# Kernel optimization log

Measured on AMD Instinct MI355X. Metric: run time of the kernel, lower is better.

Reference implementation:

```python
import jax, jax.numpy as jnp
import numpy as np

NEG_SLOPE = 0.2  # PyG GATConv default negative_slope
LN_EPS = 1e-5


def gat_conv(x, edge, W, a_src, a_dst, bias, concat):
    """PyG-style GATConv. edge: [2, E] (src, dst), self-loops already included."""
    H, C = a_src.shape
    n = x.shape[0]
    xh = (x @ W).reshape(n, H, C)                      # [N, H, C]
    es = jnp.einsum('nhc,hc->nh', xh, a_src)           # [N, H]
    ed = jnp.einsum('nhc,hc->nh', xh, a_dst)           # [N, H]
    src, dst = edge[0], edge[1]
    e = jax.nn.leaky_relu(es[src] + ed[dst], NEG_SLOPE)  # [E, H]
    m = jax.ops.segment_max(e, dst, num_segments=n)      # [N, H]
    m = jnp.where(jnp.isfinite(m), m, 0.0)
    w = jnp.exp(e - m[dst])                              # [E, H]
    denom = jax.ops.segment_sum(w, dst, num_segments=n)  # [N, H] (>0: self-loops)
    alpha = w / denom[dst]                               # [E, H]
    out = jax.ops.segment_sum(alpha[:, :, None] * xh[src], dst, num_segments=n)  # [N,H,C]
    out = out.reshape(n, H * C) if concat else out.mean(axis=1)
    return out + bias


def layer_norm(x, g, b):
    mu = x.mean(axis=-1, keepdims=True)
    var = ((x - mu) ** 2).mean(axis=-1, keepdims=True)
    return (x - mu) * jax.lax.rsqrt(var + LN_EPS) * g + b


def setup_inputs() -> dict:
    key = jax.random.key(0)
    ks = jax.random.split(key, 12)
    N, D_IN, HID, OUT, H = 100000, 256, 256, 64, 8
    C1 = HID // H  # 32
    E = 1600000
    x = jax.random.normal(ks[0], (N, D_IN), dtype=jnp.float32)
    edge_index = jax.random.randint(ks[1], (2, E), 0, N, dtype=jnp.int64)
    s = 0.05
    return {
        'x': x,
        'edge_index': edge_index,
        'W1': jax.random.normal(ks[2], (D_IN, HID), jnp.float32) * s,
        'a_src1': jax.random.normal(ks[3], (H, C1), jnp.float32) * s,
        'a_dst1': jax.random.normal(ks[4], (H, C1), jnp.float32) * s,
        'b1': jnp.zeros((HID,), jnp.float32),
        'g1': jnp.ones((HID,), jnp.float32),
        'be1': jnp.zeros((HID,), jnp.float32),
        'W2': jax.random.normal(ks[5], (HID, OUT), jnp.float32) * s,
        'a_src2': jax.random.normal(ks[6], (1, OUT), jnp.float32) * s,
        'a_dst2': jax.random.normal(ks[7], (1, OUT), jnp.float32) * s,
        'b2': jnp.zeros((OUT,), jnp.float32),
        'g2': jnp.ones((OUT,), jnp.float32),
        'be2': jnp.zeros((OUT,), jnp.float32),
    }


def reference(x, edge_index, W1, a_src1, a_dst1, b1, g1, be1, W2, a_src2, a_dst2, b2, g2, be2):
    # eval mode: dropout_edge and F.dropout are identity
    n = x.shape[0]
    loops = jnp.arange(n, dtype=edge_index.dtype)
    edge = jnp.concatenate([edge_index, jnp.stack([loops, loops])], axis=1)  # add self-loops
    h = gat_conv(x, edge, W1, a_src1, a_dst1, b1, concat=True)
    h = jax.nn.relu(layer_norm(h, g1, be1))
    h = gat_conv(h, edge, W2, a_src2, a_dst2, b2, concat=False)
    h = layer_norm(h, g2, be2)
    return jax.nn.log_softmax(h, axis=1)
```

## Files before the change

### kernel.cpp

```cpp
#include <hip/hip_runtime.h>
#include <math.h>

#define LRELU(v) ((v) > 0.0f ? (v) : 0.2f * (v))

typedef __bf16 bf16x8 __attribute__((ext_vector_type(8)));
typedef float f32x4 __attribute__((ext_vector_type(4)));
typedef float f32x2 __attribute__((ext_vector_type(2)));

__device__ __forceinline__ unsigned short f2bf(float f) {
    unsigned int u = __float_as_uint(f);
    u += 0x7FFF + ((u >> 16) & 1);
    return (unsigned short)(u >> 16);
}
__device__ __forceinline__ float bf2f(unsigned short s) {
    return __uint_as_float(((unsigned int)s) << 16);
}

__global__ __launch_bounds__(256) void prep_k(const float* __restrict__ W1, unsigned short* __restrict__ W1T,
                                              const float* __restrict__ W2, unsigned short* __restrict__ W2T,
                                              const int* __restrict__ edge, int* __restrict__ cnt,
                                              int* __restrict__ rank, int E) {
    int b = blockIdx.x;
    if (b < 256) {
        int i = b * 256 + threadIdx.x;
        int k = i >> 8, n = i & 255;
        W1T[(size_t)n * 256 + k] = f2bf(W1[i]);
    } else if (b < 320) {
        int i = (b - 256) * 256 + threadIdx.x;
        int k = i >> 6, n = i & 63;
        W2T[(size_t)n * 256 + k] = f2bf(W2[i]);
    } else {
        int i = (b - 320) * 256 + threadIdx.x;
        if (i < E) rank[i] = atomicAdd(&cnt[edge[E + i]], 1);
    }
}

__global__ __launch_bounds__(256) void psum_k(const int* __restrict__ cnt, int* __restrict__ bsum, int N) {
    __shared__ int wsh[4];
    int b = blockIdx.x;
    int gi = b * 1024 + threadIdx.x * 4;
    int s = 0;
    if (gi + 3 < N) {
        int4 v = *(const int4*)(cnt + gi);
        s = v.x + v.y + v.z + v.w + 4;
    } else {
        for (int j = 0; j < 4; ++j) if (gi + j < N) s += cnt[gi + j] + 1;
    }
#pragma unroll
    for (int off = 1; off < 64; off <<= 1) s += __shfl_xor(s, off, 64);
    if ((threadIdx.x & 63) == 0) wsh[threadIdx.x >> 6] = s;
    __syncthreads();
    if (threadIdx.x == 0) bsum[b] = wsh[0] + wsh[1] + wsh[2] + wsh[3];
}

__global__ void bscan_k(int* __restrict__ bsum, int B) {
    __shared__ int sh[128];
    int t = threadIdx.x;
    int v = (t < B) ? bsum[t] : 0;
    sh[t] = v;
    __syncthreads();
    for (int off = 1; off < 128; off <<= 1) {
        int u = (t >= off) ? sh[t - off] : 0;
        __syncthreads();
        sh[t] += u;
        __syncthreads();
    }
    if (t < B) bsum[t] = sh[t] - v;
}

__global__ __launch_bounds__(256) void rowptr_k(const int* __restrict__ cnt, const int* __restrict__ bsum,
                                                int* __restrict__ row_ptr, int N) {
    __shared__ int wsh[4];
    int b = blockIdx.x;
    int t = threadIdx.x;
    int gi = b * 1024 + t * 4;
    int c[4];
    int s = 0;
#pragma unroll
    for (int j = 0; j < 4; ++j) {
        int i = gi + j;
        c[j] = (i < N) ? cnt[i] + 1 : 0;
        s += c[j];
    }
    int lane = t & 63, w = t >> 6;
    int ps = s;
#pragma unroll
    for (int off = 1; off < 64; off <<= 1) {
        int u = __shfl_up(ps, off, 64);
        if (lane >= off) ps += u;
    }
    if (lane == 63) wsh[w] = ps;
    __syncthreads();
    int wbase = 0;
    for (int k = 0; k < w; ++k) wbase += wsh[k];
    int base = bsum[b] + wbase + (ps - s);
#pragma unroll
    for (int j = 0; j < 4; ++j) {
        int i = gi + j;
        if (i < N) row_ptr[i] = base;
        base += c[j];
    }
    if (N - 1 >= gi && N - 1 < gi + 4) row_ptr[N] = base;
}

__global__ void scatter_k(const int* __restrict__ edge, const int* __restrict__ row_ptr,
                          const int* __restrict__ rank, int* __restrict__ col, int E, int N) {
    int i = blockIdx.x * blockDim.x + threadIdx.x;
    if (i < E) {
        int dst = edge[E + i];
        col[row_ptr[dst] + rank[i]] = edge[i];
    } else if (i < E + N) {
        int n = i - E;
        col[row_ptr[n + 1] - 1] = n;
    }
}

__global__ __launch_bounds__(256) void gemm1f_k(const float* __restrict__ A,
                                                const unsigned short* __restrict__ BT,
                                                unsigned char* __restrict__ Q, int M) {
    constexpr int K = 256, BM = 128, BK = 32;
    __shared__ char As[BM * 80];
    __shared__ char Bs[256 * 80];
    int tid = threadIdx.x;
    int m0 = blockIdx.x * BM;
    int wid = tid >> 6, lane = tid & 63;
    int wm = (wid >> 1) * 64, wn = (wid & 1) * 128;
    int l15 = lane & 15, g = lane >> 4;
    f32x4 acc[4][8] = {};

    for (int k0 = 0; k0 < K; k0 += BK) {
#pragma unroll
        for (int i = 0; i < 2; ++i) {
            int c = tid + i * 256;
            int r = c >> 2, kc = c & 3;
            int gm = m0 + r; if (gm >= M) gm = M - 1;
            const float* src = A + (size_t)gm * K + k0 + kc * 8;
            float4 v0 = *(const float4*)(src);
            float4 v1 = *(const float4*)(src + 4);
            uint4 pk;
            pk.x = f2bf(v0.x) | ((unsigned)f2bf(v0.y) << 16);
            pk.y = f2bf(v0.z) | ((unsigned)f2bf(v0.w) << 16);
            pk.z = f2bf(v1.x) | ((unsigned)f2bf(v1.y) << 16);
            pk.w = f2bf(v1.z) | ((unsigned)f2bf(v1.w) << 16);
            *(uint4*)(As + r * 80 + kc * 16) = pk;
        }
#pragma unroll
        for (int i = 0; i < 4; ++i) {
            int c = tid + i * 256;
            int r = c >> 2, kc = c & 3;
            float4 v = *(const float4*)(BT + (size_t)r * K + k0 + kc * 8);
            *(float4*)(Bs + r * 80 + kc * 16) = v;
        }
        __syncthreads();
        bf16x8 af[4], bfr[8];
#pragma unroll
        for (int i = 0; i < 4; ++i)
            af[i] = *(const bf16x8*)(As + (wm + i * 16 + l15) * 80 + g * 16);
#pragma unroll
        for (int j = 0; j < 8; ++j)
            bfr[j] = *(const bf16x8*)(Bs + (wn + j * 16 + l15) * 80 + g * 16);
#pragma unroll
        for (int i = 0; i < 4; ++i)
#pragma unroll
            for (int j = 0; j < 8; ++j)
                acc[i][j] = __builtin_amdgcn_mfma_f32_16x16x32_bf16(af[i], bfr[j], acc[i][j], 0, 0, 0);
        __syncthreads();
    }
#pragma unroll
    for (int i = 0; i < 4; ++i)
#pragma unroll
        for (int j = 0; j < 8; ++j) {
            int col = wn + j * 16 + l15;
            int gmb = m0 + wm + i * 16 + g * 4;
            int p01 = __builtin_amdgcn_cvt_pk_fp8_f32(acc[i][j][0], acc[i][j][1], 0, false);
            int p23 = __builtin_amdgcn_cvt_pk_fp8_f32(acc[i][j][2], acc[i][j][3], 0, false);
#pragma unroll
            for (int r = 0; r < 4; ++r) {
                int gm = gmb + r;
                if (gm < M) {
                    int pk = (r < 2) ? p01 : p23;
                    Q[(size_t)gm * 256 + col] = (unsigned char)((pk >> ((r & 1) * 8)) & 0xff);
                }
            }
        }
}

__global__ __launch_bounds__(256) void gemm2_k(const unsigned short* __restrict__ A,
                                               const unsigned short* __restrict__ BT,
                                               unsigned char* __restrict__ Q2, int M) {
    constexpr int N = 64, K = 256, BM = 128, BK = 32, BN = 64;
    __shared__ char As[BM * 80];
    __shared__ char Bs[BN * 80];
    int tid = threadIdx.x;
    int m0 = blockIdx.x * BM;
    int wid = tid >> 6, lane = tid & 63;
    int wm = (wid >> 1) * 64, wn = (wid & 1) * 32;
    int l15 = lane & 15, g = lane >> 4;
    f32x4 acc[4][2] = {};

    for (int k0 = 0; k0 < K; k0 += BK) {
#pragma unroll
        for (int i = 0; i < 2; ++i) {
            int c = tid + i * 256;
            int r = c >> 2, kc = c & 3;
            int gm = m0 + r; if (gm >= M) gm = M - 1;
            float4 v = *(const float4*)(A + (size_t)gm * K + k0 + kc * 8);
            *(float4*)(As + r * 80 + kc * 16) = v;
        }
        {
            int c = tid;
            int r = c >> 2, kc = c & 3;
            float4 v = *(const float4*)(BT + (size_t)r * K + k0 + kc * 8);
            *(float4*)(Bs + r * 80 + kc * 16) = v;
        }
        __syncthreads();
        bf16x8 af[4], bfr[2];
#pragma unroll
        for (int i = 0; i < 4; ++i)
            af[i] = *(const bf16x8*)(As + (wm + i * 16 + l15) * 80 + g * 16);
#pragma unroll
        for (int j = 0; j < 2; ++j)
            bfr[j] = *(const bf16x8*)(Bs + (wn + j * 16 + l15) * 80 + g * 16);
#pragma unroll
        for (int i = 0; i < 4; ++i)
#pragma unroll
            for (int j = 0; j < 2; ++j)
                acc[i][j] = __builtin_amdgcn_mfma_f32_16x16x32_bf16(af[i], bfr[j], acc[i][j], 0, 0, 0);
        __syncthreads();
    }
#pragma unroll
    for (int i = 0; i < 4; ++i)
#pragma unroll
        for (int j = 0; j < 2; ++j) {
            int col = wn + j * 16 + l15;
            int gmb = m0 + wm + i * 16 + g * 4;
            int p01 = __builtin_amdgcn_cvt_pk_fp8_f32(acc[i][j][0], acc[i][j][1], 0, false);
            int p23 = __builtin_amdgcn_cvt_pk_fp8_f32(acc[i][j][2], acc[i][j][3], 0, false);
#pragma unroll
            for (int r = 0; r < 4; ++r) {
                int gm = gmb + r;
                if (gm < M) {
                    int pk = (r < 2) ? p01 : p23;
                    Q2[(size_t)gm * N + col] = (unsigned char)((pk >> ((r & 1) * 8)) & 0xff);
                }
            }
        }
}

__global__ void dots1_k(const unsigned char* __restrict__ xq, const float* __restrict__ as_,
                        const float* __restrict__ ad_, float* __restrict__ es,
                        float* __restrict__ ed, int N8) {
    __shared__ float ws[256], wd[256];
    ws[threadIdx.x] = as_[threadIdx.x];
    wd[threadIdx.x] = ad_[threadIdx.x];
    __syncthreads();
    int idx = blockIdx.x * 256 + threadIdx.x;
    if (idx >= N8) return;
    int n = idx >> 3, hh = idx & 7;
    const uint4* p = (const uint4*)(xq + (size_t)n * 256 + hh * 32);
    const float* s = ws + hh * 32;
    const float* d = wd + hh * 32;
    float a = 0.f, b = 0.f;
#pragma unroll
    for (int j = 0; j < 2; ++j) {
        uint4 v = p[j];
        unsigned dws[4] = {v.x, v.y, v.z, v.w};
#pragma unroll
        for (int k = 0; k < 4; ++k) {
            int c0 = j * 16 + k * 4;
            f32x2 lo = __builtin_amdgcn_cvt_pk_f32_fp8(dws[k], false);
            f32x2 hi = __builtin_amdgcn_cvt_pk_f32_fp8(dws[k], true);
            a += lo[0] * s[c0] + lo[1] * s[c0 + 1] + hi[0] * s[c0 + 2] + hi[1] * s[c0 + 3];
            b += lo[0] * d[c0] + lo[1] * d[c0 + 1] + hi[0] * d[c0 + 2] + hi[1] * d[c0 + 3];
        }
    }
    es[idx] = a;
    ed[idx] = b;
}

__global__ void dots2_k(const unsigned char* __restrict__ xq2, const float* __restrict__ as_,
                        const float* __restrict__ ad_, float* __restrict__ es,
                        float* __restrict__ ed, int N) {
    __shared__ float ws[64], wd[64];
    if (threadIdx.x < 64) { ws[threadIdx.x] = as_[threadIdx.x]; wd[threadIdx.x] = ad_[threadIdx.x]; }
    __syncthreads();
    int n = blockIdx.x * blockDim.x + threadIdx.x;
    if (n >= N) return;
    const uint4* p = (const uint4*)(xq2 + (size_t)n * 64);
    float a = 0.f, b = 0.f;
#pragma unroll
    for (int j = 0; j < 4; ++j) {
        uint4 v = p[j];
        unsigned dws[4] = {v.x, v.y, v.z, v.w};
#pragma unroll
        for (int k = 0; k < 4; ++k) {
            int c0 = j * 16 + k * 4;
            f32x2 lo = __builtin_amdgcn_cvt_pk_f32_fp8(dws[k], false);
            f32x2 hi = __builtin_amdgcn_cvt_pk_f32_fp8(dws[k], true);
            a += lo[0] * ws[c0] + lo[1] * ws[c0 + 1] + hi[0] * ws[c0 + 2] + hi[1] * ws[c0 + 3];
            b += lo[0] * wd[c0] + lo[1] * wd[c0 + 1] + hi[0] * wd[c0 + 2] + hi[1] * wd[c0 + 3];
        }
    }
    es[n] = a;
    ed[n] = b;
}

__global__ __launch_bounds__(256) void agg1_k(const unsigned char* __restrict__ xq,
                                              const float* __restrict__ es, const float* __restrict__ ed,
                                              const int* __restrict__ row_ptr, const int* __restrict__ col,
                                              const float* __restrict__ bias, const float* __restrict__ gam,
                                              const float* __restrict__ bet,
                                              unsigned short* __restrict__ hout, int N) {
    int tid = threadIdx.x, wid = tid >> 6, lane = tid & 63;
    int node = blockIdx.x * 4 + wid;
    if (node >= N) return;
    int half = lane >> 5, li = lane & 31;
    unsigned hh = (unsigned)(li >> 2);
    unsigned lib = (unsigned)(li * 8);
    int start = row_ptr[node];
    int deg = row_ptr[node + 1] - start;
    float edh = ed[((unsigned)node << 3) + hh];
    f32x2 acc2[4] = {};
    float wsum = 0.f;

    float esA = 0.f, esB = 0.f, esC = 0.f;
    uint2 xA = {0, 0}, xB = {0, 0}, xC = {0, 0};
    int e = half;
    if (e < deg) { unsigned src = (unsigned)col[start + e];
        esA = es[(src << 3) + hh]; xA = *(const uint2*)(xq + ((src << 8) | lib)); }
    if (e + 2 < deg) { unsigned src = (unsigned)col[start + e + 2];
        esB = es[(src << 3) + hh]; xB = *(const uint2*)(xq + ((src << 8) | lib)); }
    if (e + 4 < deg) { unsigned src = (unsigned)col[start + e + 4];
        esC = es[(src << 3) + hh]; xC = *(const uint2*)(xq + ((src << 8) | lib)); }

#define AGG1_STEP(ESB, XB)                                                        \
    {                                                                             \
        float wgt = __expf(LRELU(ESB + edh));                                     \
        wsum += wgt;                                                              \
        f32x2 w2 = {wgt, wgt};                                                    \
        acc2[0] += w2 * __builtin_amdgcn_cvt_pk_f32_fp8(XB.x, false);             \
        acc2[1] += w2 * __builtin_amdgcn_cvt_pk_f32_fp8(XB.x, true);              \
        acc2[2] += w2 * __builtin_amdgcn_cvt_pk_f32_fp8(XB.y, false);             \
        acc2[3] += w2 * __builtin_amdgcn_cvt_pk_f32_fp8(XB.y, true);              \
        if (e + 6 < deg) {                                                        \
            unsigned src = (unsigned)col[start + e + 6];                          \
            ESB = es[(src << 3) + hh];                                            \
            XB = *(const uint2*)(xq + ((src << 8) | lib));                        \
        }                                                                         \
        e += 2;                                                                   \
    }

    if (e < deg) {
        for (;;) {
            AGG1_STEP(esA, xA);
            if (e >= deg) break;
            AGG1_STEP(esB, xB);
            if (e >= deg) break;
            AGG1_STEP(esC, xC);
            if (e >= deg) break;
        }
    }
#undef AGG1_STEP

    float a8[8];
#pragma unroll
    for (int k = 0; k < 4; ++k) { a8[2 * k] = acc2[k][0]; a8[2 * k + 1] = acc2[k][1]; }
#pragma unroll
    for (int j = 0; j < 8; ++j) a8[j] += __shfl_xor(a8[j], 32, 64);
    wsum += __shfl_xor(wsum, 32, 64);
    float inv = 1.f / wsum;
    float4 bA = *(const float4*)(bias + li * 8);
    float4 bB = *(const float4*)(bias + li * 8 + 4);
    float v[8];
    v[0] = a8[0] * inv + bA.x; v[1] = a8[1] * inv + bA.y;
    v[2] = a8[2] * inv + bA.z; v[3] = a8[3] * inv + bA.w;
    v[4] = a8[4] * inv + bB.x; v[5] = a8[5] * inv + bB.y;
    v[6] = a8[6] * inv + bB.z; v[7] = a8[7] * inv + bB.w;
    float s = 0.f, q = 0.f;
#pragma unroll
    for (int j = 0; j < 8; ++j) { s += v[j]; q += v[j] * v[j]; }
#pragma unroll
    for (int off = 1; off < 32; off <<= 1) { s += __shfl_xor(s, off, 64); q += __shfl_xor(q, off, 64); }
    float mu = s * (1.f / 256.f);
    float var = q * (1.f / 256.f) - mu * mu;
    float rs = rsqrtf(var + 1e-5f);
    float4 gA = *(const float4*)(gam + li * 8);
    float4 gB = *(const float4*)(gam + li * 8 + 4);
    float4 eA = *(const float4*)(bet + li * 8);
    float4 eB = *(const float4*)(bet + li * 8 + 4);
    float o0 = fmaxf((v[0] - mu) * rs * gA.x + eA.x, 0.f);
    float o1 = fmaxf((v[1] - mu) * rs * gA.y + eA.y, 0.f);
    float o2 = fmaxf((v[2] - mu) * rs * gA.z + eA.z, 0.f);
    float o3 = fmaxf((v[3] - mu) * rs * gA.w + eA.w, 0.f);
    float o4 = fmaxf((v[4] - mu) * rs * gB.x + eB.x, 0.f);
    float o5 = fmaxf((v[5] - mu) * rs * gB.y + eB.y, 0.f);
    float o6 = fmaxf((v[6] - mu) * rs * gB.z + eB.z, 0.f);
    float o7 = fmaxf((v[7] - mu) * rs * gB.w + eB.w, 0.f);
    if (half == 0) {
        uint4 pk;
        pk.x = f2bf(o0) | ((unsigned)f2bf(o1) << 16);
        pk.y = f2bf(o2) | ((unsigned)f2bf(o3) << 16);
        pk.z = f2bf(o4) | ((unsigned)f2bf(o5) << 16);
        pk.w = f2bf(o6) | ((unsigned)f2bf(o7) << 16);
        *(uint4*)(hout + (size_t)node * 256 + li * 8) = pk;
    }
}

__global__ __launch_bounds__(256) void agg2_k(const unsigned char* __restrict__ xq2,
                                              const float* __restrict__ es, const float* __restrict__ ed,
                                              const int* __restrict__ row_ptr, const int* __restrict__ col,
                                              const float* __restrict__ bias, const float* __restrict__ gam,
                                              const float* __restrict__ bet,
                                              float* __restrict__ out, int N) {
    int tid = threadIdx.x, wid = tid >> 6, lane = tid & 63;
    int node = blockIdx.x * 4 + wid;
    if (node >= N) return;
    int g = lane >> 3, li = lane & 7;
    unsigned lib = (unsigned)(li * 8);
    int start = row_ptr[node];
    int deg = row_ptr[node + 1] - start;
    float edh = ed[node];
    f32x2 acc2[4] = {};
    float wsum = 0.f;

    float esA = 0.f, esB = 0.f, esC = 0.f;
    uint2 xA = {0, 0}, xB = {0, 0}, xC = {0, 0};
    int e = g;
    if (e < deg) { unsigned src = (unsigned)col[start + e];
        esA = es[src]; xA = *(const uint2*)(xq2 + ((src << 6) | lib)); }
    if (e + 8 < deg) { unsigned src = (unsigned)col[start + e + 8];
        esB = es[src]; xB = *(const uint2*)(xq2 + ((src << 6) | lib)); }
    if (e + 16 < deg) { unsigned src = (unsigned)col[start + e + 16];
        esC = es[src]; xC = *(const uint2*)(xq2 + ((src << 6) | lib)); }

#define AGG2_STEP(ESB, XB)                                                        \
    {                                                                             \
        float wgt = __expf(LRELU(ESB + edh));                                     \
        wsum += wgt;                                                              \
        f32x2 w2 = {wgt, wgt};                                                    \
        acc2[0] += w2 * __builtin_amdgcn_cvt_pk_f32_fp8(XB.x, false);             \
        acc2[1] += w2 * __builtin_amdgcn_cvt_pk_f32_fp8(XB.x, true);              \
        acc2[2] += w2 * __builtin_amdgcn_cvt_pk_f32_fp8(XB.y, false);             \
        acc2[3] += w2 * __builtin_amdgcn_cvt_pk_f32_fp8(XB.y, true);              \
        if (e + 24 < deg) {                                                       \
            unsigned src = (unsigned)col[start + e + 24];                         \
            ESB = es[src];                                                        \
            XB = *(const uint2*)(xq2 + ((src << 6) | lib));                       \
        }                                                                         \
        e += 8;                                                                   \
    }

    if (e < deg) {
        for (;;) {
            AGG2_STEP(esA, xA);
            if (e >= deg) break;
            AGG2_STEP(esB, xB);
            if (e >= deg) break;
            AGG2_STEP(esC, xC);
            if (e >= deg) break;
        }
    }
#undef AGG2_STEP

    float a8[8];
#pragma unroll
    for (int k = 0; k < 4; ++k) { a8[2 * k] = acc2[k][0]; a8[2 * k + 1] = acc2[k][1]; }
#pragma unroll
    for (int off = 8; off < 64; off <<= 1) {
#pragma unroll
        for (int j = 0; j < 8; ++j) a8[j] += __shfl_xor(a8[j], off, 64);
        wsum += __shfl_xor(wsum, off, 64);
    }
    int c = li * 8;
    float inv = 1.f / wsum;
    float v[8];
#pragma unroll
    for (int j = 0; j < 8; ++j) v[j] = a8[j] * inv + bias[c + j];
    float s = 0.f, q = 0.f;
#pragma unroll
    for (int j = 0; j < 8; ++j) { s += v[j]; q += v[j] * v[j]; }
#pragma unroll
    for (int off = 1; off < 8; off <<= 1) { s += __shfl_xor(s, off, 64); q += __shfl_xor(q, off, 64); }
    float mu = s * (1.f / 64.f);
    float var = q * (1.f / 64.f) - mu * mu;
    float rs = rsqrtf(var + 1e-5f);
    float o[8];
    float mx = -1e30f;
#pragma unroll
    for (int j = 0; j < 8; ++j) {
        o[j] = (v[j] - mu) * rs * gam[c + j] + bet[c + j];
        mx = fmaxf(mx, o[j]);
    }
#pragma unroll
    for (int off = 1; off < 8; off <<= 1) mx = fmaxf(mx, __shfl_xor(mx, off, 64));
    float se = 0.f;
#pragma unroll
    for (int j = 0; j < 8; ++j) se += __expf(o[j] - mx);
#pragma unroll
    for (int off = 1; off < 8; off <<= 1) se += __shfl_xor(se, off, 64);
    float lse = mx + logf(se);
    if (g == 0) {
        float4 o0 = make_float4(o[0] - lse, o[1] - lse, o[2] - lse, o[3] - lse);
        float4 o1 = make_float4(o[4] - lse, o[5] - lse, o[6] - lse, o[7] - lse);
        *(float4*)(out + (size_t)node * 64 + c) = o0;
        *(float4*)(out + (size_t)node * 64 + c + 4) = o1;
    }
}

extern "C" void kernel_launch(void* const* d_in, const int* in_sizes, int n_in,
                              void* d_out, int out_size, void* d_ws, size_t ws_size,
                              hipStream_t stream) {
    const float* x   = (const float*)d_in[0];
    const int*   edge = (const int*)d_in[1];
    const float* W1  = (const float*)d_in[2];
    const float* as1 = (const float*)d_in[3];
    const float* ad1 = (const float*)d_in[4];
    const float* b1  = (const float*)d_in[5];
    const float* g1  = (const float*)d_in[6];
    const float* be1 = (const float*)d_in[7];
    const float* W2  = (const float*)d_in[8];
    const float* as2 = (const float*)d_in[9];
    const float* ad2 = (const float*)d_in[10];
    const float* b2  = (const float*)d_in[11];
    const float* g2  = (const float*)d_in[12];
    const float* be2 = (const float*)d_in[13];

    int NN = in_sizes[0] / 256;
    int E  = in_sizes[1] / 2;
    int ET = E + NN;

    char* w = (char*)d_ws;
    size_t off = 0;
    auto nxt = [&](size_t b) -> void* {
        void* p = w + off;
        off = (off + b + 255) & ~(size_t)255;
        return p;
    };
    unsigned short* W1T  = (unsigned short*)nxt(256 * 256 * 2);
    unsigned short* W2T  = (unsigned short*)nxt(64 * 256 * 2);
    unsigned char*  xq   = (unsigned char*)nxt((size_t)NN * 256);
    unsigned short* hbuf = (unsigned short*)nxt((size_t)NN * 256 * 2);
    unsigned char*  xq2  = (unsigned char*)nxt((size_t)NN * 64);
    float* es1   = (float*)nxt((size_t)NN * 8 * 4);
    float* ed1   = (float*)nxt((size_t)NN * 8 * 4);
    float* es2   = (float*)nxt((size_t)NN * 4);
    float* ed2   = (float*)nxt((size_t)NN * 4);
    int* row_ptr = (int*)nxt((size_t)(NN + 1) * 4);
    int* tmpN    = (int*)nxt((size_t)NN * 4);
    int* rank    = (int*)nxt((size_t)E * 4);
    int* col     = (int*)nxt((size_t)ET * 4);
    int* bsum    = (int*)nxt(1024 * 4);
    (void)ws_size; (void)n_in; (void)out_size;

    int NB = (NN + 1023) / 1024;

    (void)hipMemsetAsync(tmpN, 0, (size_t)NN * 4, stream);
    prep_k<<<320 + (E + 255) / 256, 256, 0, stream>>>(W1, W1T, W2, W2T, edge, tmpN, rank, E);
    psum_k<<<NB, 256, 0, stream>>>(tmpN, bsum, NN);
    bscan_k<<<1, 128, 0, stream>>>(bsum, NB);
    rowptr_k<<<NB, 256, 0, stream>>>(tmpN, bsum, row_ptr, NN);
    scatter_k<<<(ET + 255) / 256, 256, 0, stream>>>(edge, row_ptr, rank, col, E, NN);

    gemm1f_k<<<(NN + 127) / 128, 256, 0, stream>>>(x, W1T, xq, NN);
    dots1_k<<<(NN * 8 + 255) / 256, 256, 0, stream>>>(xq, as1, ad1, es1, ed1, NN * 8);
    agg1_k<<<(NN + 3) / 4, 256, 0, stream>>>(xq, es1, ed1, row_ptr, col, b1, g1, be1, hbuf, NN);

    gemm2_k<<<(NN + 127) / 128, 256, 0, stream>>>(hbuf, W2T, xq2, NN);
    dots2_k<<<(NN + 255) / 256, 256, 0, stream>>>(xq2, as2, ad2, es2, ed2, NN);
    agg2_k<<<(NN + 3) / 4, 256, 0, stream>>>(xq2, es2, ed2, row_ptr, col, b2, g2, be2,
                                             (float*)d_out, NN);
}
```

Baseline: 350.2 us.

## Load GEMM tiles via direct global-to-LDS and widen agg2 per-lane gathers

The GEMM kernels now load bf16 B (and A in gemm2) tiles with global_load_lds, which moves data straight from global memory into LDS without passing through registers. The LDS layout changes to k-chunk-major, 16-byte-per-row slots. Separately, the layer-2 aggregation kernel gives each lane 16 fp8 features via uint4 loads instead of 8, and processes 16 edges per wave step with two prefetch buffers instead of three. This means fewer, wider gathers per edge, at the cost of less prefetch depth and more registers, and the new LDS layout may cause bank conflicts.

```diff
diff --git a/kernel.cpp b/kernel.cpp
--- a/kernel.cpp
+++ b/kernel.cpp
@@ -6,14 +6,17 @@
 typedef __bf16 bf16x8 __attribute__((ext_vector_type(8)));
 typedef float f32x4 __attribute__((ext_vector_type(4)));
 typedef float f32x2 __attribute__((ext_vector_type(2)));
+
+typedef const __attribute__((address_space(1))) unsigned int* gp_t;
+typedef __attribute__((address_space(3))) unsigned int* lp_t;
+__device__ __forceinline__ void gl16(const void* g, void* l) {
+    __builtin_amdgcn_global_load_lds((gp_t)g, (lp_t)l, 16, 0, 0);
+}
 
 __device__ __forceinline__ unsigned short f2bf(float f) {
     unsigned int u = __float_as_uint(f);
     u += 0x7FFF + ((u >> 16) & 1);
     return (unsigned short)(u >> 16);
-}
-__device__ __forceinline__ float bf2f(unsigned short s) {
-    return __uint_as_float(((unsigned int)s) << 16);
 }
 
 __global__ __launch_bounds__(256) void prep_k(const float* __restrict__ W1, unsigned short* __restrict__ W1T,
@@ -120,15 +123,22 @@
                                                 unsigned char* __restrict__ Q, int M) {
     constexpr int K = 256, BM = 128, BK = 32;
     __shared__ char As[BM * 80];
-    __shared__ char Bs[256 * 80];
+    __shared__ char Bs[4 * 256 * 16];
     int tid = threadIdx.x;
     int m0 = blockIdx.x * BM;
     int wid = tid >> 6, lane = tid & 63;
     int wm = (wid >> 1) * 64, wn = (wid & 1) * 128;
     int l15 = lane & 15, g = lane >> 4;
+    int wbase = tid & ~63;
     f32x4 acc[4][8] = {};
 
     for (int k0 = 0; k0 < K; k0 += BK) {
+#pragma unroll
+        for (int i = 0; i < 4; ++i) {
+            int c = tid + i * 256;
+            int kc = c >> 8, r = c & 255;
+            gl16(BT + (size_t)r * 256 + k0 + kc * 8, Bs + (size_t)(wbase + i * 256) * 16);
+        }
 #pragma unroll
         for (int i = 0; i < 2; ++i) {
             int c = tid + i * 256;
@@ -144,13 +154,6 @@
             pk.w = f2bf(v1.z) | ((unsigned)f2bf(v1.w) << 16);
             *(uint4*)(As + r * 80 + kc * 16) = pk;
         }
-#pragma unroll
-        for (int i = 0; i < 4; ++i) {
-            int c = tid + i * 256;
-            int r = c >> 2, kc = c & 3;
-            float4 v = *(const float4*)(BT + (size_t)r * K + k0 + kc * 8);
-            *(float4*)(Bs + r * 80 + kc * 16) = v;
-        }
         __syncthreads();
         bf16x8 af[4], bfr[8];
 #pragma unroll
@@ -158,7 +161,7 @@
             af[i] = *(const bf16x8*)(As + (wm + i * 16 + l15) * 80 + g * 16);
 #pragma unroll
         for (int j = 0; j < 8; ++j)
-            bfr[j] = *(const bf16x8*)(Bs + (wn + j * 16 + l15) * 80 + g * 16);
+            bfr[j] = *(const bf16x8*)(Bs + (size_t)((g << 8) + wn + j * 16 + l15) * 16);
 #pragma unroll
         for (int i = 0; i < 4; ++i)
 #pragma unroll
@@ -189,38 +192,37 @@
                                                const unsigned short* __restrict__ BT,
                                                unsigned char* __restrict__ Q2, int M) {
     constexpr int N = 64, K = 256, BM = 128, BK = 32, BN = 64;
-    __shared__ char As[BM * 80];
-    __shared__ char Bs[BN * 80];
+    __shared__ char As[4 * 128 * 16];
+    __shared__ char Bs[4 * 64 * 16];
     int tid = threadIdx.x;
     int m0 = blockIdx.x * BM;
     int wid = tid >> 6, lane = tid & 63;
     int wm = (wid >> 1) * 64, wn = (wid & 1) * 32;
     int l15 = lane & 15, g = lane >> 4;
+    int wbase = tid & ~63;
     f32x4 acc[4][2] = {};
 
     for (int k0 = 0; k0 < K; k0 += BK) {
 #pragma unroll
         for (int i = 0; i < 2; ++i) {
             int c = tid + i * 256;
-            int r = c >> 2, kc = c & 3;
+            int kc = c >> 7, r = c & 127;
             int gm = m0 + r; if (gm >= M) gm = M - 1;
-            float4 v = *(const float4*)(A + (size_t)gm * K + k0 + kc * 8);
-            *(float4*)(As + r * 80 + kc * 16) = v;
+            gl16(A + (size_t)gm * 256 + k0 + kc * 8, As + (size_t)(wbase + i * 256) * 16);
         }
         {
             int c = tid;
-            int r = c >> 2, kc = c & 3;
-            float4 v = *(const float4*)(BT + (size_t)r * K + k0 + kc * 8);
-            *(float4*)(Bs + r * 80 + kc * 16) = v;
+            int kc = c >> 6, r = c & 63;
+            gl16(BT + (size_t)r * 256 + k0 + kc * 8, Bs + (size_t)wbase * 16);
         }
         __syncthreads();
         bf16x8 af[4], bfr[2];
 #pragma unroll
         for (int i = 0; i < 4; ++i)
-            af[i] = *(const bf16x8*)(As + (wm + i * 16 + l15) * 80 + g * 16);
+            af[i] = *(const bf16x8*)(As + (size_t)((g << 7) + wm + i * 16 + l15) * 16);
 #pragma unroll
         for (int j = 0; j < 2; ++j)
-            bfr[j] = *(const bf16x8*)(Bs + (wn + j * 16 + l15) * 80 + g * 16);
+            bfr[j] = *(const bf16x8*)(Bs + (size_t)((g << 6) + wn + j * 16 + l15) * 16);
 #pragma unroll
         for (int i = 0; i < 4; ++i)
 #pragma unroll
@@ -415,23 +417,21 @@
     int tid = threadIdx.x, wid = tid >> 6, lane = tid & 63;
     int node = blockIdx.x * 4 + wid;
     if (node >= N) return;
-    int g = lane >> 3, li = lane & 7;
-    unsigned lib = (unsigned)(li * 8);
+    int g = lane >> 2, li = lane & 3;
+    unsigned lib = (unsigned)(li * 16);
     int start = row_ptr[node];
     int deg = row_ptr[node + 1] - start;
     float edh = ed[node];
-    f32x2 acc2[4] = {};
+    f32x2 acc2[8] = {};
     float wsum = 0.f;
 
-    float esA = 0.f, esB = 0.f, esC = 0.f;
-    uint2 xA = {0, 0}, xB = {0, 0}, xC = {0, 0};
+    float esA = 0.f, esB = 0.f;
+    uint4 xA = {0, 0, 0, 0}, xB = {0, 0, 0, 0};
     int e = g;
     if (e < deg) { unsigned src = (unsigned)col[start + e];
-        esA = es[src]; xA = *(const uint2*)(xq2 + ((src << 6) | lib)); }
-    if (e + 8 < deg) { unsigned src = (unsigned)col[start + e + 8];
-        esB = es[src]; xB = *(const uint2*)(xq2 + ((src << 6) | lib)); }
+        esA = es[src]; xA = *(const uint4*)(xq2 + ((src << 6) | lib)); }
     if (e + 16 < deg) { unsigned src = (unsigned)col[start + e + 16];
-        esC = es[src]; xC = *(const uint2*)(xq2 + ((src << 6) | lib)); }
+        esB = es[src]; xB = *(const uint4*)(xq2 + ((src << 6) | lib)); }
 
 #define AGG2_STEP(ESB, XB)                                                        \
     {                                                                             \
@@ -442,12 +442,16 @@
         acc2[1] += w2 * __builtin_amdgcn_cvt_pk_f32_fp8(XB.x, true);              \
         acc2[2] += w2 * __builtin_amdgcn_cvt_pk_f32_fp8(XB.y, false);             \
         acc2[3] += w2 * __builtin_amdgcn_cvt_pk_f32_fp8(XB.y, true);              \
-        if (e + 24 < deg) {                                                       \
-            unsigned src = (unsigned)col[start + e + 24];                         \
+        acc2[4] += w2 * __builtin_amdgcn_cvt_pk_f32_fp8(XB.z, false);             \
+        acc2[5] += w2 * __builtin_amdgcn_cvt_pk_f32_fp8(XB.z, true);              \
+        acc2[6] += w2 * __builtin_amdgcn_cvt_pk_f32_fp8(XB.w, false);             \
+        acc2[7] += w2 * __builtin_amdgcn_cvt_pk_f32_fp8(XB.w, true);              \
+        if (e + 32 < deg) {                                                       \
+            unsigned src = (unsigned)col[start + e + 32];                         \
             ESB = es[src];                                                        \
-            XB = *(const uint2*)(xq2 + ((src << 6) | lib));                       \
+            XB = *(const uint4*)(xq2 + ((src << 6) | lib));                       \
         }                                                                         \
-        e += 8;                                                                   \
+        e += 16;                                                                  \
     }
 
     if (e < deg) {
@@ -456,54 +460,54 @@
             if (e >= deg) break;
             AGG2_STEP(esB, xB);
             if (e >= deg) break;
-            AGG2_STEP(esC, xC);
-            if (e >= deg) break;
         }
     }
 #undef AGG2_STEP
 
-    float a8[8];
-#pragma unroll
-    for (int k = 0; k < 4; ++k) { a8[2 * k] = acc2[k][0]; a8[2 * k + 1] = acc2[k][1]; }
-#pragma unroll
-    for (int off = 8; off < 64; off <<= 1) {
-#pragma unroll
-        for (int j = 0; j < 8; ++j) a8[j] += __shfl_xor(a8[j], off, 64);
+    float a16[16];
+#pragma unroll
+    for (int k = 0; k < 8; ++k) { a16[2 * k] = acc2[k][0]; a16[2 * k + 1] = acc2[k][1]; }
+#pragma unroll
+    for (int off = 4; off < 64; off <<= 1) {
+#pragma unroll
+        for (int j = 0; j < 16; ++j) a16[j] += __shfl_xor(a16[j], off, 64);
         wsum += __shfl_xor(wsum, off, 64);
     }
-    int c = li * 8;
+    int c = li * 16;
     float inv = 1.f / wsum;
-    float v[8];
-#pragma unroll
-    for (int j = 0; j < 8; ++j) v[j] = a8[j] * inv + bias[c + j];
+    float v[16];
+#pragma unroll
+    for (int j = 0; j < 16; ++j) v[j] = a16[j] * inv + bias[c + j];
     float s = 0.f, q = 0.f;
 #pragma unroll
-    for (int j = 0; j < 8; ++j) { s += v[j]; q += v[j] * v[j]; }
-#pragma unroll
-    for (int off = 1; off < 8; off <<= 1) { s += __shfl_xor(s, off, 64); q += __shfl_xor(q, off, 64); }
+    for (int j = 0; j < 16; ++j) { s += v[j]; q += v[j] * v[j]; }
+#pragma unroll
+    for (int off = 1; off < 4; off <<= 1) { s += __shfl_xor(s, off, 64); q += __shfl_xor(q, off, 64); }
     float mu = s * (1.f / 64.f);
     float var = q * (1.f / 64.f) - mu * mu;
     float rs = rsqrtf(var + 1e-5f);
-    float o[8];
+    float o[16];
     float mx = -1e30f;
 #pragma unroll
-    for (int j = 0; j < 8; ++j) {
+    for (int j = 0; j < 16; ++j) {
         o[j] = (v[j] - mu) * rs * gam[c + j] + bet[c + j];
         mx = fmaxf(mx, o[j]);
     }
 #pragma unroll
-    for (int off = 1; off < 8; off <<= 1) mx = fmaxf(mx, __shfl_xor(mx, off, 64));
+    for (int off = 1; off < 4; off <<= 1) mx = fmaxf(mx, __shfl_xor(mx, off, 64));
     float se = 0.f;
 #pragma unroll
-    for (int j = 0; j < 8; ++j) se += __expf(o[j] - mx);
-#pragma unroll
-    for (int off = 1; off < 8; off <<= 1) se += __shfl_xor(se, off, 64);
+    for (int j = 0; j < 16; ++j) se += __expf(o[j] - mx);
+#pragma unroll
+    for (int off = 1; off < 4; off <<= 1) se += __shfl_xor(se, off, 64);
     float lse = mx + logf(se);
     if (g == 0) {
-        float4 o0 = make_float4(o[0] - lse, o[1] - lse, o[2] - lse, o[3] - lse);
-        float4 o1 = make_float4(o[4] - lse, o[5] - lse, o[6] - lse, o[7] - lse);
-        *(float4*)(out + (size_t)node * 64 + c) = o0;
-        *(float4*)(out + (size_t)node * 64 + c + 4) = o1;
+#pragma unroll
+        for (int k = 0; k < 4; ++k) {
+            float4 ov = make_float4(o[4 * k] - lse, o[4 * k + 1] - lse,
+                                    o[4 * k + 2] - lse, o[4 * k + 3] - lse);
+            *(float4*)(out + (size_t)node * 64 + c + 4 * k) = ov;
+        }
     }
 }
 
```

New measurement: 393.8 us. 1.12x slower.
